# Kernel optimization log

Hardware: AMD Instinct MI355X
Metric: run time of the kernel (lower is better)

Reference implementation:

```python
import jax, jax.numpy as jnp
import numpy as np

B = 16          # batch
C = 3           # num_classes
A = 9           # anchors per location
IMG = 1024.0    # image spatial size (square)
FEAT = [128, 64, 32, 16, 8]
STRIDES = [8, 16, 32, 64, 128]
BASE = [32, 64, 128, 256, 512]
TOPK = 1000     # topk_candidates_per_level
SCORE_TH = 0.05
NMS_TH = 0.5
DETS = 300      # detections_per_img
CLIP = float(np.log(1000.0 / 16.0))  # torchvision bbox_xform_clip


def _make_anchors(fs, stride, base):
    scales = np.array([1.0, 2 ** (1 / 3), 2 ** (2 / 3)])
    ratios = np.array([0.5, 1.0, 2.0])
    ws = (base * scales[None, :] / np.sqrt(ratios)[:, None]).reshape(-1)  # [9]
    hs = (base * scales[None, :] * np.sqrt(ratios)[:, None]).reshape(-1)
    cy, cx = np.meshgrid(np.arange(fs), np.arange(fs), indexing='ij')
    cx = (cx.reshape(-1, 1) + 0.5) * stride
    cy = (cy.reshape(-1, 1) + 0.5) * stride
    a = np.stack([cx - ws / 2, cy - hs / 2, cx + ws / 2, cy + hs / 2], axis=-1)
    return a.reshape(-1, 4).astype(np.float32)  # [fs*fs*A, 4] xyxy, location-major


def setup_inputs() -> dict:
    key = jax.random.key(0)
    ks = jax.random.split(key, 10)
    inp = {}
    for i, fs in enumerate(FEAT):
        inp[f'cls_l{i}'] = jax.random.normal(ks[i], (B, C * A, fs, fs), jnp.float32)
        inp[f'reg_l{i}'] = jax.random.normal(ks[5 + i], (B, 4 * A, fs, fs), jnp.float32) * 0.5
        inp[f'anchors_l{i}'] = jnp.asarray(_make_anchors(fs, STRIDES[i], BASE[i]))
    return inp


def _decode(reg, anchors):
    # BoxCoder.decode with weights (1,1,1,1): reg [K,4], anchors [K,4] xyxy
    wa = anchors[:, 2] - anchors[:, 0]
    ha = anchors[:, 3] - anchors[:, 1]
    cxa = anchors[:, 0] + 0.5 * wa
    cya = anchors[:, 1] + 0.5 * ha
    dx, dy, dw, dh = reg[:, 0], reg[:, 1], reg[:, 2], reg[:, 3]
    dw = jnp.minimum(dw, CLIP)
    dh = jnp.minimum(dh, CLIP)
    cx = dx * wa + cxa
    cy = dy * ha + cya
    w = jnp.exp(dw) * wa
    h = jnp.exp(dh) * ha
    b = jnp.stack([cx - 0.5 * w, cy - 0.5 * h, cx + 0.5 * w, cy + 0.5 * h], axis=-1)
    return jnp.clip(b, 0.0, IMG)  # clip boxes to image


def _level_select(cls_map, reg_map, anchors):
    # cls_map [C*A,H,W] -> [HWA,C]; reg_map [4A,H,W] -> [HWA,4]
    H, W = cls_map.shape[-2:]
    cls = cls_map.reshape(A, C, H, W).transpose(2, 3, 0, 1).reshape(-1, C)
    reg = reg_map.reshape(A, 4, H, W).transpose(2, 3, 0, 1).reshape(-1, 4)
    scores = jax.nn.sigmoid(cls).reshape(-1)  # [HWA*C]
    scores = jnp.where(scores > SCORE_TH, scores, 0.0)  # score threshold (mask, fixed shape)
    top_s, top_i = jax.lax.top_k(scores, TOPK)
    a_idx = top_i // C
    labels = (top_i % C).astype(jnp.int32)
    boxes = _decode(reg[a_idx], anchors[a_idx])
    return boxes, top_s, labels


def _iou1(box, boxes):
    lt = jnp.maximum(box[:2], boxes[:, :2])
    rb = jnp.minimum(box[2:], boxes[:, 2:])
    wh = jnp.clip(rb - lt, 0.0)
    inter = wh[:, 0] * wh[:, 1]
    a1 = (box[2] - box[0]) * (box[3] - box[1])
    a2 = (boxes[:, 2] - boxes[:, 0]) * (boxes[:, 3] - boxes[:, 1])
    return inter / (a1 + a2 - inter + 1e-7)


def _nms(boxes, scores, labels):
    # class-batched NMS via per-class coordinate offset; fixed DETS iterations
    b_off = boxes + (labels.astype(boxes.dtype) * (2.0 * IMG))[:, None]
    def step(s_work, _):
        j = jnp.argmax(s_work)
        sj = s_work[j]
        iou = _iou1(b_off[j], b_off)
        s_next = jnp.where(iou > NMS_TH, -1.0, s_work).at[j].set(-1.0)
        return s_next, (boxes[j], sj, labels[j])
    _, (ob, os, ol) = jax.lax.scan(step, scores, None, length=DETS)
    valid = os > SCORE_TH
    return (jnp.where(valid[:, None], ob, 0.0),
            jnp.where(valid, os, 0.0),
            jnp.where(valid, ol, -1))


def _per_image(c0, c1, c2, c3, c4, r0, r1, r2, r3, r4, a0, a1, a2, a3, a4):
    bs, ss, ls = [], [], []
    for cm, rm, an in zip((c0, c1, c2, c3, c4), (r0, r1, r2, r3, r4), (a0, a1, a2, a3, a4)):
        b, s, l = _level_select(cm, rm, an)
        bs.append(b); ss.append(s); ls.append(l)
    return _nms(jnp.concatenate(bs), jnp.concatenate(ss), jnp.concatenate(ls))


def reference(cls_l0, cls_l1, cls_l2, cls_l3, cls_l4,
              reg_l0, reg_l1, reg_l2, reg_l3, reg_l4,
              anchors_l0, anchors_l1, anchors_l2, anchors_l3, anchors_l4):
    f = jax.vmap(_per_image, in_axes=(0,) * 10 + (None,) * 5)
    boxes, scores, labels = f(cls_l0, cls_l1, cls_l2, cls_l3, cls_l4,
                              reg_l0, reg_l1, reg_l2, reg_l3, reg_l4,
                              anchors_l0, anchors_l1, anchors_l2, anchors_l3, anchors_l4)
    return boxes, scores, labels  # [B,300,4], [B,300], [B,300] int32
```

## Files before the change

kernel.cpp:

```cpp
#include <hip/hip_runtime.h>
#include <stdint.h>

#define NLEV  5
#define BATCH 16
#define TOPK  1000
#define DETS  300
#define KSTRIDE 8192

struct Ptrs {
  const float* cls[NLEV]; const float* reg[NLEV]; const float* anc[NLEV];
  uint64_t* topkeys; float4* boxes; unsigned char* labs; float* out;
};

__device__ __forceinline__ void stage_col(const float4* img, int col, int ch0, int chstep,
                                          int tpi, float thr, uint64_t* sm,
                                          unsigned* s_cnt, unsigned scap) {
  for (int ch = ch0; ch < 27; ch += chstep) {
    float4 v = img[(size_t)ch * tpi + col];
    float lg[4] = {v.x, v.y, v.z, v.w};
    #pragma unroll
    for (int j = 0; j < 4; ++j) {
      if (lg[j] > thr) {
        float s = 1.0f / (1.0f + expf(-lg[j]));
        unsigned idx = (unsigned)((col * 4 + j) * 27 + ch);
        uint64_t item = ((uint64_t)__float_as_uint(s) << 32) |
                        (uint64_t)(0xFFFFFFFFu - idx);
        unsigned p = atomicAdd(s_cnt, 1u);
        if (p < scap) sm[p] = item;
      }
    }
  }
}

__device__ __forceinline__ uint64_t* sort_desc_merge(uint64_t* sa, uint64_t* sb, int N) {
  int tid = threadIdx.x, lane = tid & 63, wave = tid >> 6;
  if (N == 2048) {
    uint64_t v0 = sa[(wave << 6) + lane];
    uint64_t v1 = sa[((wave + 16) << 6) + lane];
    #pragma unroll
    for (int k = 2; k <= 64; k <<= 1) {
      #pragma unroll
      for (int j = k >> 1; j > 0; j >>= 1) {
        uint64_t w0 = __shfl_xor((unsigned long long)v0, j);
        uint64_t w1 = __shfl_xor((unsigned long long)v1, j);
        bool tm = (((lane & k) == 0) != ((lane & j) != 0));
        v0 = (tm == (v0 < w0)) ? w0 : v0;
        v1 = (tm == (v1 < w1)) ? w1 : v1;
      }
    }
    sa[(wave << 6) + lane] = v0;
    sa[((wave + 16) << 6) + lane] = v1;
  } else {
    uint64_t v0 = sa[(wave << 6) + lane];
    #pragma unroll
    for (int k = 2; k <= 64; k <<= 1) {
      #pragma unroll
      for (int j = k >> 1; j > 0; j >>= 1) {
        uint64_t w0 = __shfl_xor((unsigned long long)v0, j);
        bool tm = (((lane & k) == 0) != ((lane & j) != 0));
        v0 = (tm == (v0 < w0)) ? w0 : v0;
      }
    }
    sa[(wave << 6) + lane] = v0;
  }
  __syncthreads();
  uint64_t* src = sa;
  uint64_t* dst = sb;
  int OUT = N >> 10;
  for (int R = 64; R < N; R <<= 1) {
    int p0 = tid * OUT;
    int seg = p0 / (2 * R);
    int p = p0 - seg * 2 * R;
    const uint64_t* A = src + (size_t)seg * 2 * R;
    const uint64_t* B = A + R;
    int lo = p - R; if (lo < 0) lo = 0;
    int hi = p < R ? p : R;
    while (lo < hi) {
      int mid = (lo + hi) >> 1;
      if (A[mid] >= B[p - mid - 1]) lo = mid + 1; else hi = mid;
    }
    int ai = lo, bi = p - lo;
    uint64_t o0, o1 = 0ull;
    {
      uint64_t av = (ai < R) ? A[ai] : 0ull;
      uint64_t bv = (bi < R) ? B[bi] : 0ull;
      bool takeA = (ai < R) && (bi >= R || av >= bv);
      o0 = takeA ? av : bv;
      if (takeA) ++ai; else ++bi;
    }
    if (OUT == 2) {
      uint64_t av = (ai < R) ? A[ai] : 0ull;
      uint64_t bv = (bi < R) ? B[bi] : 0ull;
      bool takeA = (ai < R) && (bi >= R || av >= bv);
      o1 = takeA ? av : bv;
    }
    uint64_t* base = dst + (size_t)seg * 2 * R;
    base[p] = o0;
    if (OUT == 2) base[p + 1] = o1;
    __syncthreads();
    uint64_t* t = src; src = dst; dst = t;
  }
  return src;
}

__global__ __launch_bounds__(1024) void k1_score_sort(Ptrs P) {
  __shared__ uint64_t sm[2048];
  __shared__ uint64_t sm2[2048];
  __shared__ unsigned s_cnt;
  int blk = blockIdx.x, tid = threadIdx.x;
  int l, b, run, N;
  if (blk < 64)       { l = 0; b = blk >> 2;   run = blk & 3; N = 1024; }
  else if (blk < 80)  { l = 1; b = blk - 64;   run = 4;       N = 2048; }
  else if (blk < 96)  { l = 2; b = blk - 80;   run = 5;       N = 2048; }
  else if (blk < 112) { l = 3; b = blk - 96;   run = 6;       N = 2048; }
  else                { l = 4; b = blk - 112;  run = 7;       N = 2048; }
  for (int i = tid; i < N; i += 1024) sm[i] = 0ull;
  if (tid == 0) s_cnt = 0;
  __syncthreads();
  if (l == 0) {
    const float4* img = (const float4*)P.cls[0] + (size_t)b * 27 * 4096;
    stage_col(img, run * 1024 + tid, 0, 1, 4096, 2.68f, sm, &s_cnt, 1024);
  } else if (l == 1) {
    const float4* img = (const float4*)P.cls[1] + (size_t)b * 27 * 1024;
    stage_col(img, tid, 0, 1, 1024, 2.20f, sm, &s_cnt, 2048);
  } else if (l == 2) {
    const float4* img = (const float4*)P.cls[2] + (size_t)b * 27 * 256;
    stage_col(img, tid & 255, tid >> 8, 4, 256, 1.62f, sm, &s_cnt, 2048);
  } else if (l == 3) {
    const float4* img = (const float4*)P.cls[3] + (size_t)b * 27 * 64;
    stage_col(img, tid & 63, tid >> 6, 16, 64, 0.85f, sm, &s_cnt, 2048);
  } else {
    if (tid < 432) {
      int ch = tid >> 4, col = tid & 15;
      const float4* img = (const float4*)P.cls[4] + (size_t)b * 27 * 16;
      float4 v = img[(size_t)ch * 16 + col];
      float lg[4] = {v.x, v.y, v.z, v.w};
      #pragma unroll
      for (int j = 0; j < 4; ++j) {
        float s = 1.0f / (1.0f + expf(-lg[j]));
        unsigned sb = (s > 0.05f) ? __float_as_uint(s) : 0u;
        unsigned idx = (unsigned)((col * 4 + j) * 27 + ch);
        sm[idx] = ((uint64_t)sb << 32) | (uint64_t)(0xFFFFFFFFu - idx);
      }
    }
  }
  __syncthreads();
  uint64_t* sorted = sort_desc_merge(sm, sm2, N);
  int emit = (l == 0) ? 1024 : TOPK;
  uint64_t v = (tid < emit) ? sorted[tid] : 0ull;
  int pos = (run << 10) + tid;
  uint64_t key = 0ull;
  if (v != 0ull) {
    unsigned sb = (unsigned)(v >> 32);
    key = ((uint64_t)sb << 13) | (uint64_t)(8191 - pos);
  }
  P.topkeys[(size_t)b * KSTRIDE + pos] = key;
  float4 raw = make_float4(0.f, 0.f, 0.f, 0.f);
  unsigned char lab = 0;
  if (v != 0ull) {
    unsigned idx = 0xFFFFFFFFu - (unsigned)(v & 0xFFFFFFFFull);
    int a_idx = (int)(idx / 3u);
    lab = (unsigned char)(idx - (unsigned)a_idx * 3u);
    int cell = a_idx / 9;
    int anch = a_idx - cell * 9;
    int HW = (128 >> l) * (128 >> l);
    const float* rg = P.reg[l] + ((size_t)b * 36 + (size_t)anch * 4) * HW + cell;
    float dx = rg[0];
    float dy = rg[(size_t)HW];
    float dw = rg[2 * (size_t)HW];
    float dh = rg[3 * (size_t)HW];
    float4 a4 = *(const float4*)(P.anc[l] + (size_t)a_idx * 4);
    float wa = a4.z - a4.x, ha = a4.w - a4.y;
    float cxa = a4.x + 0.5f * wa, cya = a4.y + 0.5f * ha;
    const float CLIPF = 4.135166556742356f;
    float dwc = fminf(dw, CLIPF), dhc = fminf(dh, CLIPF);
    float cx = dx * wa + cxa, cy = dy * ha + cya;
    float w = expf(dwc) * wa, h = expf(dhc) * ha;
    raw.x = fminf(fmaxf(cx - 0.5f * w, 0.f), 1024.f);
    raw.y = fminf(fmaxf(cy - 0.5f * h, 0.f), 1024.f);
    raw.z = fminf(fmaxf(cx + 0.5f * w, 0.f), 1024.f);
    raw.w = fminf(fmaxf(cy + 0.5f * h, 0.f), 1024.f);
  }
  P.boxes[(size_t)b * KSTRIDE + pos] = raw;
  P.labs [(size_t)b * KSTRIDE + pos] = lab;
}

__global__ __launch_bounds__(1024) void k2_merge_nms(Ptrs P) {
  __shared__ uint64_t sm[8192];
  __shared__ float4 kq[DETS + 4];
  __shared__ float  ka[DETS + 4];
  __shared__ unsigned long long s_mask[16];
  __shared__ unsigned long long s_adj[64];
  __shared__ int s_kcnt, s_total, s_done;
  int b = blockIdx.x, tid = threadIdx.x, wave = tid >> 6, lane = tid & 63;

  for (int i = tid; i < 8192; i += 1024)
    sm[i] = P.topkeys[(size_t)b * KSTRIDE + i];
  __syncthreads();

  for (int r = 0; r < 3; ++r) {
    int R = 1024 << r;
    int p0 = tid * 8;
    int seg = p0 / (2 * R);
    int p = p0 - seg * 2 * R;
    uint64_t* A = sm + (size_t)seg * 2 * R;
    uint64_t* B = A + R;
    int lo = p - R; if (lo < 0) lo = 0;
    int hi = p < R ? p : R;
    while (lo < hi) {
      int mid = (lo + hi) >> 1;
      if (A[mid] >= B[p - mid - 1]) lo = mid + 1; else hi = mid;
    }
    int ai = lo, bi = p - lo;
    uint64_t out[8];
    #pragma unroll
    for (int e = 0; e < 8; ++e) {
      uint64_t av = (ai < R) ? A[ai] : 0ull;
      uint64_t bv = (bi < R) ? B[bi] : 0ull;
      bool takeA = (ai < R) && (bi >= R || av >= bv);
      out[e] = takeA ? av : bv;
      if (takeA) ++ai; else ++bi;
    }
    __syncthreads();
    #pragma unroll
    for (int e = 0; e < 8; ++e) sm[(size_t)seg * 2 * R + p + e] = out[e];
    __syncthreads();
    if (r == 1) {
      for (int i = 1000 + tid; i < 4096; i += 1024) sm[i] = 0ull;
      __syncthreads();
    }
  }
  if (tid == 0) { s_kcnt = 0; s_total = 0; s_done = 0; }
  __syncthreads();

  const float4* gB = P.boxes + (size_t)b * KSTRIDE;
  const unsigned char* gL = P.labs + (size_t)b * KSTRIDE;
  float* oB = P.out + (size_t)b * DETS * 4;
  float* oS = P.out + (size_t)BATCH * DETS * 4 + (size_t)b * DETS;
  float* oL = P.out + (size_t)BATCH * DETS * 5 + (size_t)b * DETS;

  float4 bxA, bxB; int lbA, lbB;
  {
    int posA = 8191 - (int)(sm[lane] & 0x1FFF);
    bxA = gB[posA]; lbA = (int)gL[posA];
    int posB = 8191 - (int)(sm[64 + lane] & 0x1FFF);
    bxB = gB[posB]; lbB = (int)gL[posB];
  }

  for (int c = 0; c < 80; ++c) {
    float4 rb; int lb2;
    if ((c & 1) == 0) { rb = bxA; lb2 = lbA; } else { rb = bxB; lb2 = lbB; }
    if (c + 2 < 80) {
      int pos = 8191 - (int)(sm[((c + 2) << 6) + lane] & 0x1FFF);
      if ((c & 1) == 0) { bxA = gB[pos]; lbA = (int)gL[pos]; }
      else              { bxB = gB[pos]; lbB = (int)gL[pos]; }
    }
    uint64_t key = sm[(c << 6) + lane];
    float sc2 = __uint_as_float((unsigned)(key >> 13));
    bool valid = sc2 > 0.05f;
    float off = (float)lb2 * 2048.0f;
    float q0 = rb.x + off, q1 = rb.y + off, q2 = rb.z + off, q3 = rb.w + off;
    float ca = (q2 - q0) * (q3 - q1);
    bool sup = false;
    int kc = s_kcnt;
    for (int m = wave; m < kc; m += 16) {
      float4 kv = kq[m]; float kav = ka[m];
      float ltx = fmaxf(kv.x, q0), lty = fmaxf(kv.y, q1);
      float rbx = fminf(kv.z, q2), rby = fminf(kv.w, q3);
      float w = fmaxf(rbx - ltx, 0.f), h = fmaxf(rby - lty, 0.f);
      float inter = w * h;
      float iou = inter / (((kav + ca) - inter) + 1e-7f);
      sup = sup || (iou > 0.5f);
    }
    unsigned long long pm = __ballot(sup);
    if (lane == 0) s_mask[wave] = pm;
    #pragma unroll
    for (int rr = 0; rr < 4; ++rr) {
      int j = (wave << 2) | rr;
      float j0 = __shfl(q0, j), j1 = __shfl(q1, j);
      float j2 = __shfl(q2, j), j3 = __shfl(q3, j);
      float ja = __shfl(ca, j);
      float ltx = fmaxf(j0, q0), lty = fmaxf(j1, q1);
      float rbx = fminf(j2, q2), rby = fminf(j3, q3);
      float w = fmaxf(rbx - ltx, 0.f), h = fmaxf(rby - lty, 0.f);
      float inter = w * h;
      float iou = inter / (((ja + ca) - inter) + 1e-7f);
      unsigned long long am = __ballot(iou > 0.5f);
      if (lane == 0) s_adj[j] = am;
    }
    asm volatile("s_waitcnt lgkmcnt(0)" ::: "memory");
    __builtin_amdgcn_s_barrier();
    if (wave == 0) {
      unsigned long long S = 0ull;
      #pragma unroll
      for (int w2 = 0; w2 < 16; ++w2) S |= s_mask[w2];
      unsigned long long row = s_adj[lane];
      int rl = (int)(unsigned)row;
      int rh = (int)(unsigned)(row >> 32);
      unsigned long long validm = __ballot(valid);
      int kcnt0 = s_kcnt, total0 = s_total;
      unsigned long long A = validm & ~S;
      int vrank = -1, pops = 0, tot = total0;
      while (A != 0ull && tot < DETS) {
        int j = (int)__builtin_ctzll(A);
        if (lane == j) vrank = pops;
        unsigned long long rowj =
            ((unsigned long long)(unsigned)__builtin_amdgcn_readlane(rh, j) << 32) |
            (unsigned)__builtin_amdgcn_readlane(rl, j);
        A &= ~rowj;
        A &= ~(1ull << j);
        ++pops; ++tot;
      }
      if (vrank >= 0) {
        int ks = kcnt0 + vrank;
        kq[ks] = make_float4(q0, q1, q2, q3);
        ka[ks] = ca;
        int r = total0 + vrank;
        oB[4 * r + 0] = rb.x; oB[4 * r + 1] = rb.y;
        oB[4 * r + 2] = rb.z; oB[4 * r + 3] = rb.w;
        oS[r] = sc2; oL[r] = (float)lb2;
      }
      if (lane == 0) {
        s_kcnt = kcnt0 + pops; s_total = tot;
        if (tot >= DETS || validm != ~0ull) s_done = 1;
      }
    }
    asm volatile("s_waitcnt lgkmcnt(0)" ::: "memory");
    __builtin_amdgcn_s_barrier();
    if (s_done) break;
  }
  int K = s_total < DETS ? s_total : DETS;
  for (int r = K + tid; r < DETS; r += 1024) {
    oB[4 * r + 0] = 0.f; oB[4 * r + 1] = 0.f;
    oB[4 * r + 2] = 0.f; oB[4 * r + 3] = 0.f;
    oS[r] = 0.f; oL[r] = -1.0f;
  }
}

extern "C" void kernel_launch(void* const* d_in, const int* in_sizes, int n_in,
                              void* d_out, int out_size, void* d_ws, size_t ws_size,
                              hipStream_t stream) {
  Ptrs P;
  if (in_sizes[1] == 9437184) {
    for (int l = 0; l < NLEV; ++l) {
      P.cls[l] = (const float*)d_in[3 * l + 0];
      P.reg[l] = (const float*)d_in[3 * l + 1];
      P.anc[l] = (const float*)d_in[3 * l + 2];
    }
  } else {
    for (int l = 0; l < NLEV; ++l) {
      P.cls[l] = (const float*)d_in[l];
      P.reg[l] = (const float*)d_in[5 + l];
      P.anc[l] = (const float*)d_in[10 + l];
    }
  }
  char* ws = (char*)d_ws;
  P.topkeys = (uint64_t*)ws;
  P.boxes   = (float4*)(ws + (1 << 20));
  P.labs    = (unsigned char*)(ws + 3 * (1 << 20));
  P.out     = (float*)d_out;

  k1_score_sort<<<128, 1024, 0, stream>>>(P);
  k2_merge_nms <<<BATCH, 1024, 0, stream>>>(P);
}
```

Measured before the change: 220.0 us.

## Process two 64-candidate chunks per NMS iteration to halve block barriers

The greedy NMS loop now handles an even and an odd chunk of 64 candidates per iteration, so it needs half as many block-wide barriers. Wave 0 resolves the even chunk first, then tests each newly kept even box against the odd chunk through readlane before resolving the odd chunk. The stored per-box area array is dropped, and areas are recomputed from the kept boxes. The cost is more register pressure and serial work in wave 0, and some wasted work when processing stops after the even chunk.

```diff
diff --git a/kernel.cpp b/kernel.cpp
--- a/kernel.cpp
+++ b/kernel.cpp
@@ -188,9 +188,8 @@
 __global__ __launch_bounds__(1024) void k2_merge_nms(Ptrs P) {
   __shared__ uint64_t sm[8192];
   __shared__ float4 kq[DETS + 4];
-  __shared__ float  ka[DETS + 4];
-  __shared__ unsigned long long s_mask[16];
-  __shared__ unsigned long long s_adj[64];
+  __shared__ unsigned long long s_maskE[16], s_maskO[16];
+  __shared__ unsigned long long s_adjE[64], s_adjO[64];
   __shared__ int s_kcnt, s_total, s_done;
   int b = blockIdx.x, tid = threadIdx.x, wave = tid >> 6, lane = tid & 63;
 
@@ -247,82 +246,158 @@
     bxB = gB[posB]; lbB = (int)gL[posB];
   }
 
-  for (int c = 0; c < 80; ++c) {
-    float4 rb; int lb2;
-    if ((c & 1) == 0) { rb = bxA; lb2 = lbA; } else { rb = bxB; lb2 = lbB; }
-    if (c + 2 < 80) {
-      int pos = 8191 - (int)(sm[((c + 2) << 6) + lane] & 0x1FFF);
-      if ((c & 1) == 0) { bxA = gB[pos]; lbA = (int)gL[pos]; }
-      else              { bxB = gB[pos]; lbB = (int)gL[pos]; }
-    }
-    uint64_t key = sm[(c << 6) + lane];
-    float sc2 = __uint_as_float((unsigned)(key >> 13));
-    bool valid = sc2 > 0.05f;
-    float off = (float)lb2 * 2048.0f;
-    float q0 = rb.x + off, q1 = rb.y + off, q2 = rb.z + off, q3 = rb.w + off;
-    float ca = (q2 - q0) * (q3 - q1);
-    bool sup = false;
+  for (int p = 0; p < 40; ++p) {
+    int c0 = p << 1, c1 = c0 | 1;
+    float4 rbE = bxA, rbO = bxB;
+    int lbE = lbA, lbO = lbB;
+    if (c0 + 2 < 80) {
+      int pos = 8191 - (int)(sm[((c0 + 2) << 6) + lane] & 0x1FFF);
+      bxA = gB[pos]; lbA = (int)gL[pos];
+      pos = 8191 - (int)(sm[((c1 + 2) << 6) + lane] & 0x1FFF);
+      bxB = gB[pos]; lbB = (int)gL[pos];
+    }
+    uint64_t keyE = sm[(c0 << 6) + lane];
+    uint64_t keyO = sm[(c1 << 6) + lane];
+    float scE = __uint_as_float((unsigned)(keyE >> 13));
+    float scO = __uint_as_float((unsigned)(keyO >> 13));
+    bool validE = scE > 0.05f, validO = scO > 0.05f;
+    float offE = (float)lbE * 2048.0f;
+    float qE0 = rbE.x + offE, qE1 = rbE.y + offE, qE2 = rbE.z + offE, qE3 = rbE.w + offE;
+    float caE = (qE2 - qE0) * (qE3 - qE1);
+    float offO = (float)lbO * 2048.0f;
+    float qO0 = rbO.x + offO, qO1 = rbO.y + offO, qO2 = rbO.z + offO, qO3 = rbO.w + offO;
+    float caO = (qO2 - qO0) * (qO3 - qO1);
+    bool supE = false, supO = false;
     int kc = s_kcnt;
     for (int m = wave; m < kc; m += 16) {
-      float4 kv = kq[m]; float kav = ka[m];
-      float ltx = fmaxf(kv.x, q0), lty = fmaxf(kv.y, q1);
-      float rbx = fminf(kv.z, q2), rby = fminf(kv.w, q3);
-      float w = fmaxf(rbx - ltx, 0.f), h = fmaxf(rby - lty, 0.f);
-      float inter = w * h;
-      float iou = inter / (((kav + ca) - inter) + 1e-7f);
-      sup = sup || (iou > 0.5f);
-    }
-    unsigned long long pm = __ballot(sup);
-    if (lane == 0) s_mask[wave] = pm;
+      float4 kv = kq[m];
+      float kav = (kv.z - kv.x) * (kv.w - kv.y);
+      {
+        float ltx = fmaxf(kv.x, qE0), lty = fmaxf(kv.y, qE1);
+        float rbx = fminf(kv.z, qE2), rby = fminf(kv.w, qE3);
+        float w = fmaxf(rbx - ltx, 0.f), h = fmaxf(rby - lty, 0.f);
+        float inter = w * h;
+        float iou = inter / (((kav + caE) - inter) + 1e-7f);
+        supE = supE || (iou > 0.5f);
+      }
+      {
+        float ltx = fmaxf(kv.x, qO0), lty = fmaxf(kv.y, qO1);
+        float rbx = fminf(kv.z, qO2), rby = fminf(kv.w, qO3);
+        float w = fmaxf(rbx - ltx, 0.f), h = fmaxf(rby - lty, 0.f);
+        float inter = w * h;
+        float iou = inter / (((kav + caO) - inter) + 1e-7f);
+        supO = supO || (iou > 0.5f);
+      }
+    }
+    unsigned long long pmE = __ballot(supE);
+    unsigned long long pmO = __ballot(supO);
+    if (lane == 0) { s_maskE[wave] = pmE; s_maskO[wave] = pmO; }
     #pragma unroll
     for (int rr = 0; rr < 4; ++rr) {
       int j = (wave << 2) | rr;
-      float j0 = __shfl(q0, j), j1 = __shfl(q1, j);
-      float j2 = __shfl(q2, j), j3 = __shfl(q3, j);
-      float ja = __shfl(ca, j);
-      float ltx = fmaxf(j0, q0), lty = fmaxf(j1, q1);
-      float rbx = fminf(j2, q2), rby = fminf(j3, q3);
-      float w = fmaxf(rbx - ltx, 0.f), h = fmaxf(rby - lty, 0.f);
-      float inter = w * h;
-      float iou = inter / (((ja + ca) - inter) + 1e-7f);
-      unsigned long long am = __ballot(iou > 0.5f);
-      if (lane == 0) s_adj[j] = am;
+      {
+        float j0 = __shfl(qE0, j), j1 = __shfl(qE1, j);
+        float j2 = __shfl(qE2, j), j3 = __shfl(qE3, j);
+        float ja = __shfl(caE, j);
+        float ltx = fmaxf(j0, qE0), lty = fmaxf(j1, qE1);
+        float rbx = fminf(j2, qE2), rby = fminf(j3, qE3);
+        float w = fmaxf(rbx - ltx, 0.f), h = fmaxf(rby - lty, 0.f);
+        float inter = w * h;
+        float iou = inter / (((ja + caE) - inter) + 1e-7f);
+        unsigned long long am = __ballot(iou > 0.5f);
+        if (lane == 0) s_adjE[j] = am;
+      }
+      {
+        float j0 = __shfl(qO0, j), j1 = __shfl(qO1, j);
+        float j2 = __shfl(qO2, j), j3 = __shfl(qO3, j);
+        float ja = __shfl(caO, j);
+        float ltx = fmaxf(j0, qO0), lty = fmaxf(j1, qO1);
+        float rbx = fminf(j2, qO2), rby = fminf(j3, qO3);
+        float w = fmaxf(rbx - ltx, 0.f), h = fmaxf(rby - lty, 0.f);
+        float inter = w * h;
+        float iou = inter / (((ja + caO) - inter) + 1e-7f);
+        unsigned long long am = __ballot(iou > 0.5f);
+        if (lane == 0) s_adjO[j] = am;
+      }
     }
     asm volatile("s_waitcnt lgkmcnt(0)" ::: "memory");
     __builtin_amdgcn_s_barrier();
     if (wave == 0) {
       unsigned long long S = 0ull;
       #pragma unroll
-      for (int w2 = 0; w2 < 16; ++w2) S |= s_mask[w2];
-      unsigned long long row = s_adj[lane];
-      int rl = (int)(unsigned)row;
-      int rh = (int)(unsigned)(row >> 32);
-      unsigned long long validm = __ballot(valid);
+      for (int w2 = 0; w2 < 16; ++w2) S |= s_maskE[w2];
+      unsigned long long rowE = s_adjE[lane];
+      int rlE = (int)(unsigned)rowE, rhE = (int)(unsigned)(rowE >> 32);
+      int iqE0 = __float_as_int(qE0), iqE1 = __float_as_int(qE1);
+      int iqE2 = __float_as_int(qE2), iqE3 = __float_as_int(qE3);
+      int icaE = __float_as_int(caE);
+      unsigned long long validmE = __ballot(validE);
       int kcnt0 = s_kcnt, total0 = s_total;
-      unsigned long long A = validm & ~S;
-      int vrank = -1, pops = 0, tot = total0;
+      unsigned long long A = validmE & ~S;
+      int vrankE = -1, popsE = 0, tot = total0;
+      bool supOP = false;
       while (A != 0ull && tot < DETS) {
         int j = (int)__builtin_ctzll(A);
-        if (lane == j) vrank = pops;
+        if (lane == j) vrankE = popsE;
+        float k0 = __uint_as_float((unsigned)__builtin_amdgcn_readlane(iqE0, j));
+        float k1 = __uint_as_float((unsigned)__builtin_amdgcn_readlane(iqE1, j));
+        float k2 = __uint_as_float((unsigned)__builtin_amdgcn_readlane(iqE2, j));
+        float k3 = __uint_as_float((unsigned)__builtin_amdgcn_readlane(iqE3, j));
+        float kav = __uint_as_float((unsigned)__builtin_amdgcn_readlane(icaE, j));
+        float ltx = fmaxf(k0, qO0), lty = fmaxf(k1, qO1);
+        float rbx = fminf(k2, qO2), rby = fminf(k3, qO3);
+        float w = fmaxf(rbx - ltx, 0.f), h = fmaxf(rby - lty, 0.f);
+        float inter = w * h;
+        float iou = inter / (((kav + caO) - inter) + 1e-7f);
+        supOP = supOP || (iou > 0.5f);
         unsigned long long rowj =
-            ((unsigned long long)(unsigned)__builtin_amdgcn_readlane(rh, j) << 32) |
-            (unsigned)__builtin_amdgcn_readlane(rl, j);
+            ((unsigned long long)(unsigned)__builtin_amdgcn_readlane(rhE, j) << 32) |
+            (unsigned)__builtin_amdgcn_readlane(rlE, j);
         A &= ~rowj;
         A &= ~(1ull << j);
-        ++pops; ++tot;
-      }
-      if (vrank >= 0) {
-        int ks = kcnt0 + vrank;
-        kq[ks] = make_float4(q0, q1, q2, q3);
-        ka[ks] = ca;
-        int r = total0 + vrank;
-        oB[4 * r + 0] = rb.x; oB[4 * r + 1] = rb.y;
-        oB[4 * r + 2] = rb.z; oB[4 * r + 3] = rb.w;
-        oS[r] = sc2; oL[r] = (float)lb2;
+        ++popsE; ++tot;
+      }
+      if (vrankE >= 0) {
+        kq[kcnt0 + vrankE] = make_float4(qE0, qE1, qE2, qE3);
+        int r = total0 + vrankE;
+        oB[4 * r + 0] = rbE.x; oB[4 * r + 1] = rbE.y;
+        oB[4 * r + 2] = rbE.z; oB[4 * r + 3] = rbE.w;
+        oS[r] = scE; oL[r] = (float)lbE;
+      }
+      bool doneNow = (tot >= DETS) || (validmE != ~0ull);
+      int popsO = 0;
+      if (!doneNow) {
+        unsigned long long SO = 0ull;
+        #pragma unroll
+        for (int w2 = 0; w2 < 16; ++w2) SO |= s_maskO[w2];
+        SO |= __ballot(supOP);
+        unsigned long long rowO = s_adjO[lane];
+        int rlO = (int)(unsigned)rowO, rhO = (int)(unsigned)(rowO >> 32);
+        unsigned long long validmO = __ballot(validO);
+        unsigned long long AO = validmO & ~SO;
+        int vrankO = -1;
+        while (AO != 0ull && tot < DETS) {
+          int j = (int)__builtin_ctzll(AO);
+          if (lane == j) vrankO = popsO;
+          unsigned long long rowj =
+              ((unsigned long long)(unsigned)__builtin_amdgcn_readlane(rhO, j) << 32) |
+              (unsigned)__builtin_amdgcn_readlane(rlO, j);
+          AO &= ~rowj;
+          AO &= ~(1ull << j);
+          ++popsO; ++tot;
+        }
+        if (vrankO >= 0) {
+          kq[kcnt0 + popsE + vrankO] = make_float4(qO0, qO1, qO2, qO3);
+          int r = total0 + popsE + vrankO;
+          oB[4 * r + 0] = rbO.x; oB[4 * r + 1] = rbO.y;
+          oB[4 * r + 2] = rbO.z; oB[4 * r + 3] = rbO.w;
+          oS[r] = scO; oL[r] = (float)lbO;
+        }
+        if (tot >= DETS || validmO != ~0ull) doneNow = true;
       }
       if (lane == 0) {
-        s_kcnt = kcnt0 + pops; s_total = tot;
-        if (tot >= DETS || validm != ~0ull) s_done = 1;
+        s_kcnt = kcnt0 + popsE + popsO; s_total = tot;
+        if (doneNow) s_done = 1;
       }
     }
     asm volatile("s_waitcnt lgkmcnt(0)" ::: "memory");
@@ -361,5 +436,5 @@
   P.out     = (float*)d_out;
 
   k1_score_sort<<<128, 1024, 0, stream>>>(P);
-  k2_merge_nms <<<BATCH, 1024, 0, stream>>>(P);
+  k2_merge_nms<<<BATCH, 1024, 0, stream>>>(P);
 }
```

Result: slower. 235.8 us (+7.2%).
